# Kernel optimization log

Hardware: AMD Instinct MI355X
Metric: run time of the kernel (lower is better)

The kernel has to match this reference:

```python
import jax, jax.numpy as jnp
import numpy as np

BITS = 4
MASK = (1 << BITS) - 1  # 15


def _dequant(qweight, scales, qzeros, groupsize):
    # qweight: [in//32*bits, out] int32; 8 nibbles packed per int32 along rows.
    out_f = qweight.shape[1]
    shifts = jnp.arange(0, 32, BITS, dtype=jnp.int32)  # [8]
    # [rows, 8, out] -> unpacked int weights in [0, 15]
    w = (qweight[:, None, :] >> shifts[None, :, None]) & MASK
    w = w.reshape(-1, groupsize, out_f)  # [n_groups, groupsize, out]
    s = scales.reshape(-1, 1, out_f)     # [n_groups, 1, out]
    z = qzeros.reshape(-1, 1, out_f)
    W = s * w.astype(scales.dtype) - z * s
    return W.reshape(-1, out_f)          # [in, out]


def setup_inputs() -> dict:
    key = jax.random.key(0)
    k1, k2, k3, k4, k5 = jax.random.split(key, 5)
    B, S, IN, OUT, G = 4, 2048, 4096, 4096, 64
    x = jax.random.normal(k1, (B, S, IN), dtype=jnp.float16)
    qweight = jax.random.randint(k2, (IN // 32 * BITS, OUT), 0, 2147483647, dtype=jnp.int32)
    scales = (jax.random.uniform(k3, (IN // G, OUT), dtype=jnp.float32) * 0.01 + 0.001).astype(jnp.float16)
    qzeros = (jax.random.uniform(k4, (IN // G, OUT), dtype=jnp.float32) * 15.0).astype(jnp.float16)
    bias = jax.random.normal(k5, (OUT,), dtype=jnp.float16)
    return {"x": x, "qweight": qweight, "scales": scales, "qzeros": qzeros,
            "bias": bias, "groupsize": G, "bits": BITS}


def reference(x, qweight, scales, qzeros, bias, groupsize, bits):
    W = _dequant(qweight, scales, qzeros, groupsize)  # [in, out] fp16
    return jnp.matmul(x, W) + bias
```

## Files before the change

kernel.cpp:

```cpp
#include <hip/hip_runtime.h>
#include <stdint.h>
#include <stddef.h>

typedef __bf16 bf16;
typedef __bf16 bf16x8 __attribute__((ext_vector_type(8)));
typedef float  f32x4  __attribute__((ext_vector_type(4)));

#define GLOBAL_AS(p) ((const __attribute__((address_space(1))) void*)(p))
#define LDS_AS(p)    ((__attribute__((address_space(3))) void*)(p))

__device__ __forceinline__ void gload_lds16(const bf16* g, bf16* l) {
    __builtin_amdgcn_global_load_lds(GLOBAL_AS(g), LDS_AS(l), 16, 0, 0);
}

__global__ __launch_bounds__(256)
void convert_x_kernel(const float* __restrict__ x, bf16* __restrict__ xb, long n8) {
    long t = (long)blockIdx.x * blockDim.x + threadIdx.x;
    if (t >= n8) return;
    const f32x4* p = (const f32x4*)(x + t * 8);
    f32x4 a = p[0], b = p[1];
    bf16x8 v;
#pragma unroll
    for (int j = 0; j < 4; ++j) { v[j] = (bf16)a[j]; v[4 + j] = (bf16)b[j]; }
    *(bf16x8*)(xb + t * 8) = v;
}

__global__ __launch_bounds__(256)
void dequant_wt64_kernel(const uint32_t* __restrict__ qw,
                         const float* __restrict__ scales,
                         const float* __restrict__ qzeros,
                         bf16* __restrict__ Wt,
                         int N, int K, int rows_per_group) {
    const int i = blockIdx.x * 256 + threadIdx.x;
    const int w = i >> 6, l = i & 63;
    const int nr8 = K >> 6;
    const int r8 = w % nr8;
    const int o  = (w / nr8) * 8 + (l >> 3);
    const int rr = l & 7;
    const int r  = r8 * 8 + rr;
    if (o >= N) return;
    const uint32_t q = qw[(size_t)r * N + o];
    const int g = r / rows_per_group;
    const float s = scales[(size_t)g * N + o];
    const float z = qzeros[(size_t)g * N + o];
    const float nsz = -s * z;
    bf16x8 v;
#pragma unroll
    for (int j = 0; j < 8; ++j)
        v[j] = (bf16)fmaf((float)((q >> (4 * j)) & 15u), s, nsz);
    *(bf16x8*)(Wt + ((size_t)r8 * N + o) * 64 + rr * 8) = v;
}

constexpr int BM2 = 256, BN2 = 256, BK2 = 64;

#define PHASE_MID()                                      \
    __builtin_amdgcn_s_barrier();                        \
    asm volatile("s_waitcnt lgkmcnt(0)" ::: "memory");   \
    __builtin_amdgcn_sched_barrier(0);                   \
    __builtin_amdgcn_s_setprio(1)

#define PHASE_END()                                      \
    __builtin_amdgcn_s_setprio(0);                       \
    __builtin_amdgcn_sched_barrier(0);                   \
    __builtin_amdgcn_s_barrier();                        \
    __builtin_amdgcn_sched_barrier(0)

#define PHASE_END_VM4()                                  \
    __builtin_amdgcn_s_setprio(0);                       \
    __builtin_amdgcn_sched_barrier(0);                   \
    asm volatile("s_waitcnt vmcnt(4)" ::: "memory");     \
    __builtin_amdgcn_s_barrier();                        \
    __builtin_amdgcn_sched_barrier(0)

#define MFMA_HALF(A, B, IBASE)                                             \
    _Pragma("unroll")                                                      \
    for (int i_ = 0; i_ < 4; ++i_) {                                       \
        _Pragma("unroll")                                                  \
        for (int j_ = 0; j_ < 4; ++j_)                                     \
            acc[(IBASE) + i_][j_] = __builtin_amdgcn_mfma_f32_16x16x32_bf16( \
                (A)[(IBASE) + i_], (B)[j_], acc[(IBASE) + i_][j_], 0, 0, 0); \
    }

__global__ __launch_bounds__(512, 2)
void gemm8_kernel(const bf16* __restrict__ Ab,
                  const bf16* __restrict__ Bt,
                  const float* __restrict__ bias,
                  float* __restrict__ out,
                  int M, int N, int K, int nbx) {
    __shared__ __align__(16) bf16 As[2][BM2 * BK2];
    __shared__ __align__(16) bf16 Bs[2][BN2 * BK2];

    const int tid  = threadIdx.x;
    const int lane = tid & 63;
    const int wave = tid >> 6;
    const int wm = wave >> 2;
    const int wn = wave & 3;

    const int nwg = gridDim.x;
    int wg = blockIdx.x;
    {
        const int q = nwg >> 3, r = nwg & 7;
        const int xcd = wg & 7, off = wg >> 3;
        wg = (xcd < r ? xcd * (q + 1) : r * (q + 1) + (xcd - r) * q) + off;
    }
    const int nby = nwg / nbx;
    const int bx = wg / nby;
    const int by = wg % nby;
    const int m0 = by * BM2;
    const int n0 = bx * BN2;

    const int lrow = lane & 15;
    const int lhi  = lane >> 4;
    const int swz  = (lrow >> 1) & 7;

    const int NT = K >> 6;
    const int NI = NT >> 1;

    auto stageA = [&](int tIdx, int half, int buf) {
#pragma unroll
        for (int it = 0; it < 2; ++it) {
            const int q  = tid + it * 512;
            const int rl = q >> 3;
            const int cl = (q & 7) ^ ((rl >> 1) & 7);
            gload_lds16(Ab + (size_t)(m0 + half * 128 + rl) * K + tIdx * 64 + cl * 8,
                        &As[buf][half * 8192 + q * 8]);
        }
    };
    auto stageB = [&](int tIdx, int half, int buf) {
#pragma unroll
        for (int it = 0; it < 2; ++it) {
            const int q  = tid + it * 512;
            const int rl = q >> 3;
            const int cl = (q & 7) ^ ((rl >> 1) & 7);
            gload_lds16(Bt + ((size_t)tIdx * N + n0 + half * 128 + rl) * 64 + cl * 8,
                        &Bs[buf][half * 8192 + q * 8]);
        }
    };

    f32x4 acc[8][4];
#pragma unroll
    for (int i = 0; i < 8; ++i)
#pragma unroll
        for (int j = 0; j < 4; ++j) acc[i][j] = (f32x4){0.f, 0.f, 0.f, 0.f};

    stageA(0, 0, 0); stageA(0, 1, 0); stageB(0, 0, 0); stageB(0, 1, 0);
    stageA(1, 0, 1); stageA(1, 1, 1);
    asm volatile("s_waitcnt vmcnt(4)" ::: "memory");
    __builtin_amdgcn_s_barrier();
    __builtin_amdgcn_sched_barrier(0);

    bf16x8 a0[8], a1[8], b0[4], b1[4];

    for (int i2 = 0; i2 < NI; ++i2) {
        const int t0  = 2 * i2;
        const int tS2 = (t0 + 2 < NT) ? t0 + 2 : NT - 1;
        const int tS3 = (t0 + 3 < NT) ? t0 + 3 : NT - 1;

#pragma unroll
        for (int i = 0; i < 8; ++i)
            a0[i] = *(const bf16x8*)(&As[0][(wm * 128 + i * 16 + lrow) * 64 + ((lhi ^ swz) * 8)]);
#pragma unroll
        for (int j = 0; j < 4; ++j)
            b0[j] = *(const bf16x8*)(&Bs[0][(wn * 64 + j * 16 + lrow) * 64 + ((lhi ^ swz) * 8)]);
        stageB(t0 + 1, 0, 1);
        PHASE_MID();
        MFMA_HALF(a0, b0, 0);
        PHASE_END();

#pragma unroll
        for (int i = 0; i < 8; ++i)
            a1[i] = *(const bf16x8*)(&As[0][(wm * 128 + i * 16 + lrow) * 64 + (((lhi + 4) ^ swz) * 8)]);
        stageB(t0 + 1, 1, 1);
        PHASE_MID();
        MFMA_HALF(a0, b0, 4);
        PHASE_END();

#pragma unroll
        for (int j = 0; j < 4; ++j)
            b1[j] = *(const bf16x8*)(&Bs[0][(wn * 64 + j * 16 + lrow) * 64 + (((lhi + 4) ^ swz) * 8)]);
        stageA(tS2, 0, 0);
        PHASE_MID();
        MFMA_HALF(a1, b1, 0);
        PHASE_END();

        stageA(tS2, 1, 0);
        PHASE_MID();
        MFMA_HALF(a1, b1, 4);
        PHASE_END_VM4();

#pragma unroll
        for (int i = 0; i < 8; ++i)
            a0[i] = *(const bf16x8*)(&As[1][(wm * 128 + i * 16 + lrow) * 64 + ((lhi ^ swz) * 8)]);
#pragma unroll
        for (int j = 0; j < 4; ++j)
            b0[j] = *(const bf16x8*)(&Bs[1][(wn * 64 + j * 16 + lrow) * 64 + ((lhi ^ swz) * 8)]);
        stageB(tS2, 0, 0);
        PHASE_MID();
        MFMA_HALF(a0, b0, 0);
        PHASE_END();

#pragma unroll
        for (int i = 0; i < 8; ++i)
            a1[i] = *(const bf16x8*)(&As[1][(wm * 128 + i * 16 + lrow) * 64 + (((lhi + 4) ^ swz) * 8)]);
        stageB(tS2, 1, 0);
        PHASE_MID();
        MFMA_HALF(a0, b0, 4);
        PHASE_END();

#pragma unroll
        for (int j = 0; j < 4; ++j)
            b1[j] = *(const bf16x8*)(&Bs[1][(wn * 64 + j * 16 + lrow) * 64 + (((lhi + 4) ^ swz) * 8)]);
        stageA(tS3, 0, 1);
        PHASE_MID();
        MFMA_HALF(a1, b1, 0);
        PHASE_END();

        stageA(tS3, 1, 1);
        PHASE_MID();
        MFMA_HALF(a1, b1, 4);
        PHASE_END_VM4();
    }

    asm volatile("s_waitcnt vmcnt(0)" ::: "memory");

#pragma unroll
    for (int j = 0; j < 4; ++j) {
        const int col = n0 + wn * 64 + j * 16 + lrow;
        const float bv = bias[col];
#pragma unroll
        for (int i = 0; i < 8; ++i) {
            const int rbase = m0 + wm * 128 + i * 16 + lhi * 4;
#pragma unroll
            for (int r = 0; r < 4; ++r)
                out[(size_t)(rbase + r) * N + col] = acc[i][j][r] + bv;
        }
    }
}

constexpr int BM = 128, BN = 128, BK = 32;

__global__ __launch_bounds__(256)
void gemm_fused_kernel(const float* __restrict__ Af,
                       const uint32_t* __restrict__ qw,
                       const float* __restrict__ scales,
                       const float* __restrict__ qzeros,
                       const float* __restrict__ bias,
                       float* __restrict__ out,
                       int M, int N, int K, int G) {
    __shared__ __align__(16) bf16 As2[BM * BK];
    __shared__ __align__(16) bf16 Bs2[BN * BK];

    const int tid  = threadIdx.x;
    const int lane = tid & 63;
    const int wave = tid >> 6;
    const int wmm = wave & 1;
    const int wnn = wave >> 1;
    const int m0 = blockIdx.y * BM;
    const int n0 = blockIdx.x * BN;

    const int lr = lane & 15;
    const int lk8 = (lane >> 4) * 8;

    f32x4 acc[4][4];
#pragma unroll
    for (int i = 0; i < 4; ++i)
#pragma unroll
        for (int j = 0; j < 4; ++j) acc[i][j] = (f32x4){0.f, 0.f, 0.f, 0.f};

    for (int kt = 0; kt < K; kt += BK) {
#pragma unroll
        for (int it = 0; it < 2; ++it) {
            const int c = tid + it * 256;
            const int row = c >> 2;
            const int kc  = (c & 3) * 8;
            const f32x4* p = (const f32x4*)(Af + (size_t)(m0 + row) * K + kt + kc);
            f32x4 a = p[0], b = p[1];
            bf16x8 v;
#pragma unroll
            for (int j = 0; j < 4; ++j) { v[j] = (bf16)a[j]; v[4 + j] = (bf16)b[j]; }
            *(bf16x8*)(As2 + row * BK + kc) = v;
        }
        const int g = kt / G;
#pragma unroll
        for (int it = 0; it < 2; ++it) {
            const int idx = tid + it * 256;
            const int rl = idx >> 7;
            const int nl = idx & 127;
            uint32_t q = qw[(size_t)(kt / 8 + rl) * N + n0 + nl];
            float s = scales[(size_t)g * N + n0 + nl];
            float z = qzeros[(size_t)g * N + n0 + nl];
            float nsz = -s * z;
            bf16x8 v;
#pragma unroll
            for (int j = 0; j < 8; ++j)
                v[j] = (bf16)fmaf((float)((q >> (4 * j)) & 15u), s, nsz);
            *(bf16x8*)(Bs2 + nl * BK + rl * 8) = v;
        }
        __syncthreads();

        bf16x8 a[4], b[4];
#pragma unroll
        for (int i = 0; i < 4; ++i)
            a[i] = *(const bf16x8*)(As2 + (wmm * 64 + i * 16 + lr) * BK + lk8);
#pragma unroll
        for (int j = 0; j < 4; ++j)
            b[j] = *(const bf16x8*)(Bs2 + (wnn * 64 + j * 16 + lr) * BK + lk8);

#pragma unroll
        for (int i = 0; i < 4; ++i)
#pragma unroll
            for (int j = 0; j < 4; ++j)
                acc[i][j] = __builtin_amdgcn_mfma_f32_16x16x32_bf16(
                    a[i], b[j], acc[i][j], 0, 0, 0);
        __syncthreads();
    }

#pragma unroll
    for (int j = 0; j < 4; ++j) {
        const int col = n0 + wnn * 64 + j * 16 + (lane & 15);
        const float bv = bias[col];
#pragma unroll
        for (int i = 0; i < 4; ++i) {
            const int rbase = m0 + wmm * 64 + i * 16 + (lane >> 4) * 4;
#pragma unroll
            for (int r = 0; r < 4; ++r)
                out[(size_t)(rbase + r) * N + col] = acc[i][j][r] + bv;
        }
    }
}

extern "C" void kernel_launch(void* const* d_in, const int* in_sizes, int n_in,
                              void* d_out, int out_size, void* d_ws, size_t ws_size,
                              hipStream_t stream) {
    const float*    x      = (const float*)d_in[0];
    const uint32_t* qw     = (const uint32_t*)d_in[1];
    const float*    scales = (const float*)d_in[2];
    const float*    qzeros = (const float*)d_in[3];
    const float*    bias   = (const float*)d_in[4];
    float*          out    = (float*)d_out;

    const int N = in_sizes[4];
    const int K = (in_sizes[1] / N) * 8;
    const int M = in_sizes[0] / K;
    const int G = K / (in_sizes[2] / N);

    const size_t xb_bytes = (size_t)M * K * sizeof(bf16);
    const size_t wt_bytes = (size_t)N * K * sizeof(bf16);

    const bool shape_ok = (M % BM2 == 0) && (N % BN2 == 0) && (K % 128 == 0) &&
                          (G % 8 == 0);

    if (shape_ok && ws_size >= xb_bytes + wt_bytes) {
        bf16* Xb = (bf16*)d_ws;
        bf16* Wt = (bf16*)((char*)d_ws + xb_bytes);
        const long n8 = (long)M * K / 8;
        convert_x_kernel<<<(int)((n8 + 255) / 256), 256, 0, stream>>>(x, Xb, n8);
        const long dq_threads = ((long)K >> 6) * (N / 8) * 64;
        dequant_wt64_kernel<<<(int)((dq_threads + 255) / 256), 256, 0, stream>>>(
            qw, scales, qzeros, Wt, N, K, G / 8);
        const int nbx = N / BN2;
        const int nwg = nbx * (M / BM2);
        gemm8_kernel<<<nwg, 512, 0, stream>>>(Xb, Wt, bias, out, M, N, K, nbx);
    } else {
        dim3 grid(N / BN, M / BM);
        gemm_fused_kernel<<<grid, 256, 0, stream>>>(
            x, qw, scales, qzeros, bias, out, M, N, K, G);
    }
}
```

Before: 529.1 us.

## Software-pipeline LDS fragment reads one phase ahead of MFMA in GEMM loop

```diff
diff --git a/kernel.cpp b/kernel.cpp
--- a/kernel.cpp
+++ b/kernel.cpp
@@ -53,24 +53,20 @@
 
 constexpr int BM2 = 256, BN2 = 256, BK2 = 64;
 
-#define PHASE_MID()                                      \
-    __builtin_amdgcn_s_barrier();                        \
-    asm volatile("s_waitcnt lgkmcnt(0)" ::: "memory");   \
-    __builtin_amdgcn_sched_barrier(0);                   \
-    __builtin_amdgcn_s_setprio(1)
-
-#define PHASE_END()                                      \
+#define SB()    __builtin_amdgcn_sched_barrier(0)
+#define BAR()   __builtin_amdgcn_s_barrier()
+#define LGKM0() asm volatile("s_waitcnt lgkmcnt(0)" ::: "memory")
+#define VMCNT(N) asm volatile("s_waitcnt vmcnt(" #N ")" ::: "memory")
+
+#define PHASE_TAIL(A, B, IBASE)                          \
+    SB();                                                \
+    __builtin_amdgcn_s_setprio(1);                       \
+    MFMA_HALF(A, B, IBASE);                              \
     __builtin_amdgcn_s_setprio(0);                       \
-    __builtin_amdgcn_sched_barrier(0);                   \
-    __builtin_amdgcn_s_barrier();                        \
-    __builtin_amdgcn_sched_barrier(0)
-
-#define PHASE_END_VM4()                                  \
-    __builtin_amdgcn_s_setprio(0);                       \
-    __builtin_amdgcn_sched_barrier(0);                   \
-    asm volatile("s_waitcnt vmcnt(4)" ::: "memory");     \
-    __builtin_amdgcn_s_barrier();                        \
-    __builtin_amdgcn_sched_barrier(0)
+    SB();                                                \
+    LGKM0();                                             \
+    BAR();                                               \
+    SB()
 
 #define MFMA_HALF(A, B, IBASE)                                             \
     _Pragma("unroll")                                                      \
@@ -80,6 +76,17 @@
             acc[(IBASE) + i_][j_] = __builtin_amdgcn_mfma_f32_16x16x32_bf16( \
                 (A)[(IBASE) + i_], (B)[j_], acc[(IBASE) + i_][j_], 0, 0, 0); \
     }
+
+#define READ_A4(DST, BUF, KH, LO)                                          \
+    _Pragma("unroll")                                                      \
+    for (int i_ = (LO); i_ < (LO) + 4; ++i_)                               \
+        DST[i_] = *(const bf16x8*)(&As[BUF][(wm * 128 + i_ * 16 + lrow) * 64 \
+                                           + (((lhi + 4 * (KH)) ^ swz) * 8)]);
+#define READ_B4(DST, BUF, KH)                                              \
+    _Pragma("unroll")                                                      \
+    for (int j_ = 0; j_ < 4; ++j_)                                         \
+        DST[j_] = *(const bf16x8*)(&Bs[BUF][(wn * 64 + j_ * 16 + lrow) * 64 \
+                                           + (((lhi + 4 * (KH)) ^ swz) * 8)]);
 
 __global__ __launch_bounds__(512, 2)
 void gemm8_kernel(const bf16* __restrict__ Ab,
@@ -145,80 +152,63 @@
 
     stageA(0, 0, 0); stageA(0, 1, 0); stageB(0, 0, 0); stageB(0, 1, 0);
     stageA(1, 0, 1); stageA(1, 1, 1);
-    asm volatile("s_waitcnt vmcnt(4)" ::: "memory");
-    __builtin_amdgcn_s_barrier();
-    __builtin_amdgcn_sched_barrier(0);
-
-    bf16x8 a0[8], a1[8], b0[4], b1[4];
+    VMCNT(4);
+    BAR();
+    SB();
+
+    bf16x8 fa0[8], fa1[8], fb0[4], fb1[4];
+    READ_A4(fa0, 0, 0, 0);
+    READ_B4(fb0, 0, 0);
+    LGKM0();
+    SB();
 
     for (int i2 = 0; i2 < NI; ++i2) {
         const int t0  = 2 * i2;
+        const int tB1 = t0 + 1;
         const int tS2 = (t0 + 2 < NT) ? t0 + 2 : NT - 1;
         const int tS3 = (t0 + 3 < NT) ? t0 + 3 : NT - 1;
 
-#pragma unroll
-        for (int i = 0; i < 8; ++i)
-            a0[i] = *(const bf16x8*)(&As[0][(wm * 128 + i * 16 + lrow) * 64 + ((lhi ^ swz) * 8)]);
-#pragma unroll
-        for (int j = 0; j < 4; ++j)
-            b0[j] = *(const bf16x8*)(&Bs[0][(wn * 64 + j * 16 + lrow) * 64 + ((lhi ^ swz) * 8)]);
-        stageB(t0 + 1, 0, 1);
-        PHASE_MID();
-        MFMA_HALF(a0, b0, 0);
-        PHASE_END();
-
-#pragma unroll
-        for (int i = 0; i < 8; ++i)
-            a1[i] = *(const bf16x8*)(&As[0][(wm * 128 + i * 16 + lrow) * 64 + (((lhi + 4) ^ swz) * 8)]);
-        stageB(t0 + 1, 1, 1);
-        PHASE_MID();
-        MFMA_HALF(a0, b0, 4);
-        PHASE_END();
-
-#pragma unroll
-        for (int j = 0; j < 4; ++j)
-            b1[j] = *(const bf16x8*)(&Bs[0][(wn * 64 + j * 16 + lrow) * 64 + (((lhi + 4) ^ swz) * 8)]);
+        READ_A4(fa0, 0, 0, 4);
+        stageB(tB1, 0, 1);
+        stageB(tB1, 1, 1);
+        PHASE_TAIL(fa0, fb0, 0);
+
+        READ_A4(fa1, 0, 1, 0);
+        READ_B4(fb1, 0, 1);
+        PHASE_TAIL(fa0, fb0, 4);
+
+        READ_A4(fa1, 0, 1, 4);
+        stageB(tS2, 0, 0);
+        stageB(tS2, 1, 0);
+        PHASE_TAIL(fa1, fb1, 0);
+
         stageA(tS2, 0, 0);
-        PHASE_MID();
-        MFMA_HALF(a1, b1, 0);
-        PHASE_END();
-
+        VMCNT(6);
+        BAR();
+        SB();
+        READ_A4(fa0, 1, 0, 0);
+        READ_B4(fb0, 1, 0);
+        PHASE_TAIL(fa1, fb1, 4);
+
+        READ_A4(fa0, 1, 0, 4);
         stageA(tS2, 1, 0);
-        PHASE_MID();
-        MFMA_HALF(a1, b1, 4);
-        PHASE_END_VM4();
-
-#pragma unroll
-        for (int i = 0; i < 8; ++i)
-            a0[i] = *(const bf16x8*)(&As[1][(wm * 128 + i * 16 + lrow) * 64 + ((lhi ^ swz) * 8)]);
-#pragma unroll
-        for (int j = 0; j < 4; ++j)
-            b0[j] = *(const bf16x8*)(&Bs[1][(wn * 64 + j * 16 + lrow) * 64 + ((lhi ^ swz) * 8)]);
-        stageB(tS2, 0, 0);
-        PHASE_MID();
-        MFMA_HALF(a0, b0, 0);
-        PHASE_END();
-
-#pragma unroll
-        for (int i = 0; i < 8; ++i)
-            a1[i] = *(const bf16x8*)(&As[1][(wm * 128 + i * 16 + lrow) * 64 + (((lhi + 4) ^ swz) * 8)]);
-        stageB(tS2, 1, 0);
-        PHASE_MID();
-        MFMA_HALF(a0, b0, 4);
-        PHASE_END();
-
-#pragma unroll
-        for (int j = 0; j < 4; ++j)
-            b1[j] = *(const bf16x8*)(&Bs[1][(wn * 64 + j * 16 + lrow) * 64 + (((lhi + 4) ^ swz) * 8)]);
+        PHASE_TAIL(fa0, fb0, 0);
+
+        READ_A4(fa1, 1, 1, 0);
+        READ_B4(fb1, 1, 1);
+        PHASE_TAIL(fa0, fb0, 4);
+
+        READ_A4(fa1, 1, 1, 4);
+        PHASE_TAIL(fa1, fb1, 0);
+
         stageA(tS3, 0, 1);
-        PHASE_MID();
-        MFMA_HALF(a1, b1, 0);
-        PHASE_END();
-
         stageA(tS3, 1, 1);
-        PHASE_MID();
-        MFMA_HALF(a1, b1, 4);
-        PHASE_END_VM4();
+        VMCNT(4);
+        BAR();
+        SB();
+        READ_A4(fa0, 0, 0, 0);
+        READ_B4(fb0, 0, 0);
+        PHASE_TAIL(fa1, fb1, 4);
     }
 
     asm volatile("s_waitcnt vmcnt(0)" ::: "memory");
```

Measured after the change: 500.0 us. -5.5%, faster.
